# Optimization experiments

Hardware: AMD Instinct MI355X
Metric: run time of the kernel (lower is better)

The kernel has to match this reference:

```python
import jax, jax.numpy as jnp
import numpy as np

N = 150000      # active voxels
C = 64          # head input channels
KK = 9          # 3x3 kernel offsets
H = W = 700     # BEV feature map
BN_EPS = 1e-5
HEADS = [("heatmap", 3), ("center", 2), ("center_z", 1), ("dim", 3), ("rot", 2)]


def _build_neighbor_table(seed=0):
    """Submanifold 3x3 neighbor indices for N active voxels on an HxW grid.
    Entry -1 means the neighbor site is inactive (contributes zero)."""
    rng = np.random.default_rng(seed)
    flat = rng.choice(H * W, size=N, replace=False)
    ys, xs = flat // W, flat % W
    lut = np.full(H * W, -1, np.int64)
    lut[flat] = np.arange(N)
    nbr = np.full((N, KK), -1, np.int64)
    k = 0
    for dy in (-1, 0, 1):
        for dx in (-1, 0, 1):
            ny, nx = ys + dy, xs + dx
            valid = (ny >= 0) & (ny < H) & (nx >= 0) & (nx < W)
            nf = np.where(valid, ny * W + nx, 0)
            nbr[:, k] = np.where(valid, lut[nf], -1)
            k += 1
    return nbr


def setup_inputs() -> dict:
    key = jax.random.key(0)
    ks = jax.random.split(key, 2 + 2 * len(HEADS))
    inp = {
        "features": jax.random.normal(ks[0], (N, C), jnp.float32),
        "nbr_idx": jnp.asarray(_build_neighbor_table(), jnp.int32),
        # one 3x3 subm conv per head, stacked: [n_heads, 9, C_in, C_out]
        "W3": jax.random.normal(ks[1], (len(HEADS), KK, C, C), jnp.float32) * 0.05,
        "gamma": jnp.ones((len(HEADS), C), jnp.float32),
        "beta": jnp.zeros((len(HEADS), C), jnp.float32),
    }
    for i, (name, oc) in enumerate(HEADS):
        inp[f"W1_{name}"] = jax.random.normal(ks[2 + i], (C, oc), jnp.float32) * 0.001
        if name == "heatmap":
            inp[f"b1_{name}"] = jnp.full((oc,), -float(np.log((1 - 0.01) / 0.01)), jnp.float32)
        else:
            inp[f"b1_{name}"] = jnp.zeros((oc,), jnp.float32)
    return inp


def _forward(features, nbr_idx, W3, gamma, beta, W1s, b1s):
    valid = nbr_idx >= 0                                  # [N, 9]
    idx = jnp.where(valid, nbr_idx, 0)
    # gather active-neighbor features; missing neighbors -> zero (subm conv)
    gathered = features[idx] * valid[..., None].astype(features.dtype)  # [N, 9, C]
    # all heads share the same input sparse tensor -> batched gather-GEMM
    h = jnp.einsum('nkc,hkco->hno', gathered, W3)         # [n_heads, N, C]
    # BatchNorm1d (training-mode batch stats, biased var) + ReLU
    mean = h.mean(axis=1, keepdims=True)
    var = ((h - mean) ** 2).mean(axis=1, keepdims=True)
    hn = (h - mean) * jax.lax.rsqrt(var + BN_EPS)
    hn = jax.nn.relu(hn * gamma[:, None, :] + beta[:, None, :])
    # per-head 1x1 subm conv == linear on active features
    return tuple(hn[i] @ W1s[i] + b1s[i] for i in range(len(HEADS)))


def reference(features, nbr_idx, W3, gamma, beta,
              W1_heatmap, b1_heatmap, W1_center, b1_center,
              W1_center_z, b1_center_z, W1_dim, b1_dim, W1_rot, b1_rot):
    W1s = [W1_heatmap, W1_center, W1_center_z, W1_dim, W1_rot]
    b1s = [b1_heatmap, b1_center, b1_center_z, b1_dim, b1_rot]
    return _forward(features, nbr_idx, W3, gamma, beta, W1s, b1s)
```

## Files before the change

### kernel.cpp

```cpp
#include <hip/hip_runtime.h>

#define NVOX 150000
#define BM 128
#define MTILES 1172
#define SROW 150016
#define NCOL 320

typedef __attribute__((ext_vector_type(8))) short bf16x8;
typedef __attribute__((ext_vector_type(4))) float f32x4;

__device__ __forceinline__ unsigned short f2bf(float f) {
    unsigned u = __builtin_bit_cast(unsigned, f);
    u += 0x7fffu + ((u >> 16) & 1u);
    return (unsigned short)(u >> 16);
}

__device__ __forceinline__ void gld16(const void* g, void* l) {
    __builtin_amdgcn_global_load_lds(
        (const __attribute__((address_space(1))) unsigned int*)g,
        (__attribute__((address_space(3))) unsigned int*)l, 16, 0, 0);
}

__global__ void prep_feat(const float* __restrict__ src, unsigned short* __restrict__ dst) {
    int i = blockIdx.x * 256 + threadIdx.x;
    if (i < NVOX * 8) {
        const float* s = src + (size_t)i * 8;
        float4 a = *(const float4*)s;
        float4 b = *(const float4*)(s + 4);
        union { bf16x8 v; unsigned short u[8]; } r;
        r.u[0] = f2bf(a.x); r.u[1] = f2bf(a.y); r.u[2] = f2bf(a.z); r.u[3] = f2bf(a.w);
        r.u[4] = f2bf(b.x); r.u[5] = f2bf(b.y); r.u[6] = f2bf(b.z); r.u[7] = f2bf(b.w);
        *(bf16x8*)(dst + (size_t)i * 8) = r.v;
    } else if (i < NVOX * 8 + 8) {
        bf16x8 z = {0, 0, 0, 0, 0, 0, 0, 0};
        *(bf16x8*)(dst + (size_t)i * 8) = z;
    }
}

__global__ void prep_w3(const float* __restrict__ w3, unsigned short* __restrict__ bt,
                        float* __restrict__ stats) {
    int i = blockIdx.x * 256 + threadIdx.x;
    int h = i / 36864;
    int rem = i - h * 36864;
    int kk = rem >> 12;
    int c = (rem >> 6) & 63;
    int o = rem & 63;
    bt[(size_t)(((h * 9 + kk) * 8) + (c >> 3)) * 512 + o * 8 + (c & 7)] = f2bf(w3[i]);
    if (i < 2 * NCOL) stats[i] = 0.f;
}

__global__ __launch_bounds__(512, 2)
void gemm_kernel(const unsigned short* __restrict__ featB,
                 const unsigned short* __restrict__ Bt2,
                 const int* __restrict__ nbr,
                 unsigned short* __restrict__ hbuf,
                 float* __restrict__ stats,
                 float* __restrict__ partials) {
    __shared__ __align__(16) char smem[119296];
    constexpr int SB_OFF = 32768;
    constexpr int IDX_OFF = 114688;
    constexpr int SRED_OFF = 88064;

    int mtile = blockIdx.x;
    int m0 = mtile * BM;

    int tid = threadIdx.x;
    int w = tid >> 6, lane = tid & 63;
    int quad = lane >> 4, m16 = lane & 15;

    for (int lin = tid; lin < BM * 9; lin += 512) {
        int row = lin / 9, kkq = lin - row * 9;
        int v = -1;
        if (m0 + row < NVOX) v = nbr[(size_t)(m0 + row) * 9 + kkq];
        *(int*)(smem + IDX_OFF + (kkq * BM + row) * 4) = ((v < 0) ? NVOX : v) * 128;
    }
    __syncthreads();

    f32x4 acc[4][5];
#pragma unroll
    for (int mt = 0; mt < 4; ++mt)
#pragma unroll
        for (int nt = 0; nt < 5; ++nt)
            acc[mt][nt] = (f32x4){0.f, 0.f, 0.f, 0.f};

    const char* fb = (const char*)featB;
    const char* bt = (const char*)Bt2;
    char* sAb[2] = {smem, smem + 16384};
    char* sBb[2] = {smem + SB_OFF, smem + SB_OFF + 40960};

    int mrow = (w >> 2) * 64;
    int cbase = (w & 3) * 80;

    int rloc = lane >> 3, j = lane & 7;
    int jx = (j ^ rloc) * 16;

    int bsj[5], bdj[5];
#pragma unroll
    for (int jj = 0; jj < 5; ++jj) {
        int u = w * 5 + jj;
        int h = u >> 3, c16 = u & 7;
        bsj[jj] = (h * 72 + c16) * 1024 + lane * 16;
        bdj[jj] = (h * 8 + c16) * 1024;
    }
    int sBoff[5];
#pragma unroll
    for (int nt = 0; nt < 5; ++nt) {
        int c = cbase + nt * 16 + m16;
        sBoff[nt] = (c >> 6) * 8192 + (c & 63) * 16;
    }
    int aRow[4];
#pragma unroll
    for (int mt = 0; mt < 4; ++mt)
        aRow[mt] = (mrow + mt * 16 + m16) * 128;
    int axor = m16 & 7;

    auto stage = [&](int buf, int kk) {
        char* sA = sAb[buf];
        char* sB = sBb[buf];
        int off0 = *(const int*)(smem + IDX_OFF + (kk * BM + w * 16 + rloc) * 4);
        int off1 = *(const int*)(smem + IDX_OFF + (kk * BM + w * 16 + 8 + rloc) * 4);
        gld16(fb + off0 + jx, sA + w * 2048);
        gld16(fb + off1 + jx, sA + w * 2048 + 1024);
#pragma unroll
        for (int jj = 0; jj < 5; ++jj)
            gld16(bt + (size_t)(bsj[jj] + kk * 8192), sB + bdj[jj]);
    };

    stage(0, 0);

#pragma unroll
    for (int kk = 0; kk < 9; ++kk) {
        const int p = kk & 1;
        if (kk < 8) {
            stage(p ^ 1, kk + 1);
            asm volatile("s_waitcnt vmcnt(7)" ::: "memory");
        } else {
            asm volatile("s_waitcnt vmcnt(0)" ::: "memory");
        }
        asm volatile("s_barrier" ::: "memory");
        __builtin_amdgcn_sched_barrier(0);
        __builtin_amdgcn_s_setprio(1);
#pragma unroll
        for (int ks = 0; ks < 2; ++ks) {
            bf16x8 af[4], bf[5];
            int xq = ((ks * 4 + quad) ^ axor) * 16;
#pragma unroll
            for (int mt = 0; mt < 4; ++mt)
                af[mt] = *(const bf16x8*)(sAb[p] + aRow[mt] + xq);
#pragma unroll
            for (int nt = 0; nt < 5; ++nt)
                bf[nt] = *(const bf16x8*)(sBb[p] + sBoff[nt] + (ks * 4 + quad) * 1024);
#pragma unroll
            for (int mt = 0; mt < 4; ++mt)
#pragma unroll
                for (int nt = 0; nt < 5; ++nt)
                    acc[mt][nt] = __builtin_amdgcn_mfma_f32_16x16x32_bf16(
                        af[mt], bf[nt], acc[mt][nt], 0, 0, 0);
        }
        __builtin_amdgcn_s_setprio(0);
        __builtin_amdgcn_sched_barrier(0);
        asm volatile("s_barrier" ::: "memory");
    }

#pragma unroll
    for (int mt = 0; mt < 4; ++mt) {
#pragma unroll
        for (int nt = 0; nt < 5; ++nt) {
            int col = cbase + nt * 16 + m16;
            int row = mrow + mt * 16 + quad * 4;
            f32x4 v = acc[mt][nt];
            unsigned lo = (unsigned)f2bf(v.x) | ((unsigned)f2bf(v.y) << 16);
            unsigned hi = (unsigned)f2bf(v.z) | ((unsigned)f2bf(v.w) << 16);
            uint2 pk; pk.x = lo; pk.y = hi;
            *(uint2*)(smem + col * 272 + row * 2) = pk;
        }
    }
    __syncthreads();
#pragma unroll
    for (int it = 0; it < 20; ++it) {
        int col = it * 16 + (tid >> 5);
        int l32 = tid & 31;
        uint2 v = *(const uint2*)(smem + col * 272 + l32 * 8);
        *(uint2*)(hbuf + (size_t)col * SROW + m0 + l32 * 4) = v;
    }

    float s[5], ss[5];
#pragma unroll
    for (int nt = 0; nt < 5; ++nt) {
        float a = 0.f, b = 0.f;
#pragma unroll
        for (int mt = 0; mt < 4; ++mt) {
            f32x4 v = acc[mt][nt];
            a += v.x + v.y + v.z + v.w;
            b += v.x * v.x + v.y * v.y + v.z * v.z + v.w * v.w;
        }
        s[nt] = a; ss[nt] = b;
        s[nt] += __shfl_xor(s[nt], 16); s[nt] += __shfl_xor(s[nt], 32);
        ss[nt] += __shfl_xor(ss[nt], 16); ss[nt] += __shfl_xor(ss[nt], 32);
    }
    if (quad == 0) {
#pragma unroll
        for (int nt = 0; nt < 5; ++nt) {
            float* p = (float*)(smem + SRED_OFF + (w * 80 + nt * 16 + m16) * 8);
            p[0] = s[nt]; p[1] = ss[nt];
        }
    }
    __syncthreads();
    if (tid < NCOL) {
        int c = tid;
        int qq = c / 80, lc = c - qq * 80;
        const float* p0 = (const float*)(smem + SRED_OFF + (qq * 80 + lc) * 8);
        const float* p1 = (const float*)(smem + SRED_OFF + ((qq + 4) * 80 + lc) * 8);
        float vsum = p0[0] + p1[0];
        float vss  = p0[1] + p1[1];
        if (partials) {
            float* pp = partials + (size_t)mtile * (2 * NCOL);
            pp[c] = vsum;
            pp[NCOL + c] = vss;
        } else {
            atomicAdd(&stats[c], vsum);
            atomicAdd(&stats[NCOL + c], vss);
        }
    }
}

__global__ __launch_bounds__(256)
void stats_reduce(const float* __restrict__ partials, float* __restrict__ stats) {
    __shared__ float red[256];
    int b = blockIdx.x;
    int tid = threadIdx.x;
    int cl = tid & 31;
    int chunk = tid >> 5;
    int jcol = b * 32 + cl;
    float s = 0.f;
    int m1 = chunk * 147 + 147; if (m1 > MTILES) m1 = MTILES;
    for (int m = chunk * 147; m < m1; ++m)
        s += partials[(size_t)m * (2 * NCOL) + jcol];
    red[tid] = s;
    __syncthreads();
    if (tid < 32) {
        float a = red[tid];
#pragma unroll
        for (int k = 1; k < 8; ++k) a += red[k * 32 + tid];
        stats[b * 32 + tid] = a;
    }
}

__global__ __launch_bounds__(256)
void head_kernel(const unsigned short* __restrict__ hbuf,
                 const float* __restrict__ stats,
                 const float* __restrict__ gamma, const float* __restrict__ beta,
                 const float* __restrict__ W1_0, const float* __restrict__ W1_1,
                 const float* __restrict__ W1_2, const float* __restrict__ W1_3,
                 const float* __restrict__ W1_4,
                 const float* __restrict__ b1_0, const float* __restrict__ b1_1,
                 const float* __restrict__ b1_2, const float* __restrict__ b1_3,
                 const float* __restrict__ b1_4,
                 float* __restrict__ out) {
    __shared__ float sScale[64], sShift[64], sW1[192], sB1[3];
    int h = blockIdx.y;
    const float* W1; const float* b1; int oc; size_t obase;
    if (h == 0)      { W1 = W1_0; b1 = b1_0; oc = 3; obase = 0; }
    else if (h == 1) { W1 = W1_1; b1 = b1_1; oc = 2; obase = 450000; }
    else if (h == 2) { W1 = W1_2; b1 = b1_2; oc = 1; obase = 750000; }
    else if (h == 3) { W1 = W1_3; b1 = b1_3; oc = 3; obase = 900000; }
    else             { W1 = W1_4; b1 = b1_4; oc = 2; obase = 1350000; }

    int tid = threadIdx.x;
    if (tid < 64) {
        int c = h * 64 + tid;
        float mean = stats[c] * (1.f / (float)NVOX);
        float var = stats[NCOL + c] * (1.f / (float)NVOX) - mean * mean;
        float inv = rsqrtf(var + 1e-5f);
        float sc = inv * gamma[c];
        sScale[tid] = sc;
        sShift[tid] = beta[c] - mean * sc;
    }
    for (int i = tid; i < 192; i += 256) {
        int cc = i / 3, jj = i - cc * 3;
        sW1[i] = (jj < oc) ? W1[cc * oc + jj] : 0.f;
    }
    if (tid == 0) {
        sB1[0] = b1[0];
        sB1[1] = (oc >= 2) ? b1[1] : 0.f;
        sB1[2] = (oc >= 3) ? b1[2] : 0.f;
    }
    __syncthreads();

    int n = (blockIdx.x * 256 + tid) * 4;
    if (n >= NVOX) return;
    const unsigned short* hp = hbuf + (size_t)(h * 64) * SROW + n;
    float x[4][3];
#pragma unroll
    for (int rr = 0; rr < 4; ++rr) { x[rr][0] = sB1[0]; x[rr][1] = sB1[1]; x[rr][2] = sB1[2]; }
#pragma unroll 8
    for (int cc = 0; cc < 64; ++cc) {
        uint2 raw = *(const uint2*)(hp + (size_t)cc * SROW);
        float sc = sScale[cc], sh = sShift[cc];
        float w0 = sW1[cc * 3 + 0], w1 = sW1[cc * 3 + 1], w2 = sW1[cc * 3 + 2];
        float v0 = __builtin_bit_cast(float, raw.x << 16);
        float v1 = __builtin_bit_cast(float, raw.x & 0xffff0000u);
        float v2 = __builtin_bit_cast(float, raw.y << 16);
        float v3 = __builtin_bit_cast(float, raw.y & 0xffff0000u);
        v0 = fmaxf(v0 * sc + sh, 0.f); v1 = fmaxf(v1 * sc + sh, 0.f);
        v2 = fmaxf(v2 * sc + sh, 0.f); v3 = fmaxf(v3 * sc + sh, 0.f);
        x[0][0] += v0 * w0; x[0][1] += v0 * w1; x[0][2] += v0 * w2;
        x[1][0] += v1 * w0; x[1][1] += v1 * w1; x[1][2] += v1 * w2;
        x[2][0] += v2 * w0; x[2][1] += v2 * w1; x[2][2] += v2 * w2;
        x[3][0] += v3 * w0; x[3][1] += v3 * w1; x[3][2] += v3 * w2;
    }
#pragma unroll
    for (int rr = 0; rr < 4; ++rr) {
        float* op = out + obase + (size_t)(n + rr) * oc;
        op[0] = x[rr][0];
        if (oc >= 2) op[1] = x[rr][1];
        if (oc >= 3) op[2] = x[rr][2];
    }
}

extern "C" void kernel_launch(void* const* d_in, const int* in_sizes, int n_in,
                              void* d_out, int out_size, void* d_ws, size_t ws_size,
                              hipStream_t stream) {
    const float* features = (const float*)d_in[0];
    const int* nbr        = (const int*)d_in[1];
    const float* w3       = (const float*)d_in[2];
    const float* gamma    = (const float*)d_in[3];
    const float* beta     = (const float*)d_in[4];
    const float* W1_0 = (const float*)d_in[5];  const float* b1_0 = (const float*)d_in[6];
    const float* W1_1 = (const float*)d_in[7];  const float* b1_1 = (const float*)d_in[8];
    const float* W1_2 = (const float*)d_in[9];  const float* b1_2 = (const float*)d_in[10];
    const float* W1_3 = (const float*)d_in[11]; const float* b1_3 = (const float*)d_in[12];
    const float* W1_4 = (const float*)d_in[13]; const float* b1_4 = (const float*)d_in[14];
    float* out = (float*)d_out;

    char* ws = (char*)d_ws;
    unsigned short* featB = (unsigned short*)ws;
    unsigned short* Bt2   = (unsigned short*)(ws + 19200128);
    float* stats          = (float*)(ws + 19568768);
    unsigned short* hbuf  = (unsigned short*)(ws + 19571328);
    constexpr size_t PART_OFF = 19571328 + (size_t)NCOL * SROW * 2;
    float* partials = nullptr;
    if (ws_size >= PART_OFF + (size_t)MTILES * 2 * NCOL * 4)
        partials = (float*)(ws + PART_OFF);

    prep_feat<<<(NVOX * 8 + 8 + 255) / 256, 256, 0, stream>>>(features, featB);
    prep_w3<<<184320 / 256, 256, 0, stream>>>(w3, Bt2, stats);
    gemm_kernel<<<MTILES, 512, 0, stream>>>(featB, Bt2, nbr, hbuf, stats, partials);
    if (partials)
        stats_reduce<<<20, 256, 0, stream>>>(partials, stats);
    head_kernel<<<dim3(147, 5), 256, 0, stream>>>(hbuf, stats, gamma, beta,
        W1_0, W1_1, W1_2, W1_3, W1_4, b1_0, b1_1, b1_2, b1_3, b1_4, out);
}
```

Baseline: 250.8 us.

## Triple-buffer gathered A tiles, merge prep kernels, and parallelize stats reduction

The GEMM kernel now keeps three LDS buffers for the gathered feature tiles, so neighbor gathers are issued two steps ahead while the weight tiles stay double-buffered. This deepens prefetch to hide random-gather latency, at the cost of 16 KB more LDS per block, which may reduce occupancy at two blocks per CU. The two prep kernels are merged into one launch. stats_reduce now runs on a 20x8 grid and combines results with atomicAdd, relying on stats being zeroed in prep.

```diff
diff --git a/kernel.cpp b/kernel.cpp
--- a/kernel.cpp
+++ b/kernel.cpp
@@ -21,32 +21,34 @@
         (__attribute__((address_space(3))) unsigned int*)l, 16, 0, 0);
 }
 
-__global__ void prep_feat(const float* __restrict__ src, unsigned short* __restrict__ dst) {
-    int i = blockIdx.x * 256 + threadIdx.x;
-    if (i < NVOX * 8) {
-        const float* s = src + (size_t)i * 8;
-        float4 a = *(const float4*)s;
-        float4 b = *(const float4*)(s + 4);
-        union { bf16x8 v; unsigned short u[8]; } r;
-        r.u[0] = f2bf(a.x); r.u[1] = f2bf(a.y); r.u[2] = f2bf(a.z); r.u[3] = f2bf(a.w);
-        r.u[4] = f2bf(b.x); r.u[5] = f2bf(b.y); r.u[6] = f2bf(b.z); r.u[7] = f2bf(b.w);
-        *(bf16x8*)(dst + (size_t)i * 8) = r.v;
-    } else if (i < NVOX * 8 + 8) {
-        bf16x8 z = {0, 0, 0, 0, 0, 0, 0, 0};
-        *(bf16x8*)(dst + (size_t)i * 8) = z;
-    }
-}
-
-__global__ void prep_w3(const float* __restrict__ w3, unsigned short* __restrict__ bt,
-                        float* __restrict__ stats) {
-    int i = blockIdx.x * 256 + threadIdx.x;
-    int h = i / 36864;
-    int rem = i - h * 36864;
-    int kk = rem >> 12;
-    int c = (rem >> 6) & 63;
-    int o = rem & 63;
-    bt[(size_t)(((h * 9 + kk) * 8) + (c >> 3)) * 512 + o * 8 + (c & 7)] = f2bf(w3[i]);
-    if (i < 2 * NCOL) stats[i] = 0.f;
+__global__ void prep_all(const float* __restrict__ src, unsigned short* __restrict__ dst,
+                         const float* __restrict__ w3, unsigned short* __restrict__ bt,
+                         float* __restrict__ stats) {
+    int bid = blockIdx.x, tid = threadIdx.x;
+    if (bid < 4688) {
+        int i = bid * 256 + tid;
+        if (i < NVOX * 8) {
+            const float* s = src + (size_t)i * 8;
+            float4 a = *(const float4*)s;
+            float4 b = *(const float4*)(s + 4);
+            union { bf16x8 v; unsigned short u[8]; } r;
+            r.u[0] = f2bf(a.x); r.u[1] = f2bf(a.y); r.u[2] = f2bf(a.z); r.u[3] = f2bf(a.w);
+            r.u[4] = f2bf(b.x); r.u[5] = f2bf(b.y); r.u[6] = f2bf(b.z); r.u[7] = f2bf(b.w);
+            *(bf16x8*)(dst + (size_t)i * 8) = r.v;
+        } else if (i < NVOX * 8 + 8) {
+            bf16x8 z = {0, 0, 0, 0, 0, 0, 0, 0};
+            *(bf16x8*)(dst + (size_t)i * 8) = z;
+        }
+    } else {
+        int i = (bid - 4688) * 256 + tid;
+        int h = i / 36864;
+        int rem = i - h * 36864;
+        int kk = rem >> 12;
+        int c = (rem >> 6) & 63;
+        int o = rem & 63;
+        bt[(size_t)(((h * 9 + kk) * 8) + (c >> 3)) * 512 + o * 8 + (c & 7)] = f2bf(w3[i]);
+        if (i < 2 * NCOL) stats[i] = 0.f;
+    }
 }
 
 __global__ __launch_bounds__(512, 2)
@@ -56,9 +58,9 @@
                  unsigned short* __restrict__ hbuf,
                  float* __restrict__ stats,
                  float* __restrict__ partials) {
-    __shared__ __align__(16) char smem[119296];
-    constexpr int SB_OFF = 32768;
-    constexpr int IDX_OFF = 114688;
+    __shared__ __align__(16) char smem[135680];
+    constexpr int SB_OFF = 49152;
+    constexpr int IDX_OFF = 131072;
     constexpr int SRED_OFF = 88064;
 
     int mtile = blockIdx.x;
@@ -85,8 +87,6 @@
 
     const char* fb = (const char*)featB;
     const char* bt = (const char*)Bt2;
-    char* sAb[2] = {smem, smem + 16384};
-    char* sBb[2] = {smem + SB_OFF, smem + SB_OFF + 40960};
 
     int mrow = (w >> 2) * 64;
     int cbase = (w & 3) * 80;
@@ -114,42 +114,32 @@
         aRow[mt] = (mrow + mt * 16 + m16) * 128;
     int axor = m16 & 7;
 
-    auto stage = [&](int buf, int kk) {
-        char* sA = sAb[buf];
-        char* sB = sBb[buf];
+    auto stageA = [&](int buf, int kk) {
+        char* sA = smem + buf * 16384;
         int off0 = *(const int*)(smem + IDX_OFF + (kk * BM + w * 16 + rloc) * 4);
         int off1 = *(const int*)(smem + IDX_OFF + (kk * BM + w * 16 + 8 + rloc) * 4);
         gld16(fb + off0 + jx, sA + w * 2048);
         gld16(fb + off1 + jx, sA + w * 2048 + 1024);
+    };
+    auto stageB = [&](int buf, int kk) {
+        char* sB = smem + SB_OFF + buf * 40960;
 #pragma unroll
         for (int jj = 0; jj < 5; ++jj)
             gld16(bt + (size_t)(bsj[jj] + kk * 8192), sB + bdj[jj]);
     };
-
-    stage(0, 0);
-
-#pragma unroll
-    for (int kk = 0; kk < 9; ++kk) {
-        const int p = kk & 1;
-        if (kk < 8) {
-            stage(p ^ 1, kk + 1);
-            asm volatile("s_waitcnt vmcnt(7)" ::: "memory");
-        } else {
-            asm volatile("s_waitcnt vmcnt(0)" ::: "memory");
-        }
-        asm volatile("s_barrier" ::: "memory");
-        __builtin_amdgcn_sched_barrier(0);
-        __builtin_amdgcn_s_setprio(1);
+    auto computeStep = [&](int pA, int pB) {
+        const char* sA = smem + pA * 16384;
+        const char* sB = smem + SB_OFF + pB * 40960;
 #pragma unroll
         for (int ks = 0; ks < 2; ++ks) {
             bf16x8 af[4], bf[5];
             int xq = ((ks * 4 + quad) ^ axor) * 16;
 #pragma unroll
             for (int mt = 0; mt < 4; ++mt)
-                af[mt] = *(const bf16x8*)(sAb[p] + aRow[mt] + xq);
+                af[mt] = *(const bf16x8*)(sA + aRow[mt] + xq);
 #pragma unroll
             for (int nt = 0; nt < 5; ++nt)
-                bf[nt] = *(const bf16x8*)(sBb[p] + sBoff[nt] + (ks * 4 + quad) * 1024);
+                bf[nt] = *(const bf16x8*)(sB + sBoff[nt] + (ks * 4 + quad) * 1024);
 #pragma unroll
             for (int mt = 0; mt < 4; ++mt)
 #pragma unroll
@@ -157,10 +147,41 @@
                     acc[mt][nt] = __builtin_amdgcn_mfma_f32_16x16x32_bf16(
                         af[mt], bf[nt], acc[mt][nt], 0, 0, 0);
         }
-        __builtin_amdgcn_s_setprio(0);
-        __builtin_amdgcn_sched_barrier(0);
-        asm volatile("s_barrier" ::: "memory");
-    }
+    };
+
+    stageA(0, 0);
+    stageA(1, 1);
+    stageB(0, 0);
+
+#define STR2(x) #x
+#define VMCNT(N) asm volatile("s_waitcnt vmcnt(" STR2(N) ")" ::: "memory")
+#define GEMM_STEP(KK, WN)                                                   \
+    do {                                                                    \
+        if ((KK) < 8) stageB((KK + 1) & 1, (KK) + 1);                       \
+        if ((KK) < 7) stageA(((KK) + 2) % 3, (KK) + 2);                     \
+        VMCNT(WN);                                                          \
+        asm volatile("s_barrier" ::: "memory");                             \
+        __builtin_amdgcn_sched_barrier(0);                                  \
+        __builtin_amdgcn_s_setprio(1);                                      \
+        computeStep((KK) % 3, (KK) & 1);                                    \
+        __builtin_amdgcn_s_setprio(0);                                      \
+        __builtin_amdgcn_sched_barrier(0);                                  \
+        asm volatile("s_barrier" ::: "memory");                             \
+    } while (0)
+
+    GEMM_STEP(0, 7);
+    GEMM_STEP(1, 9);
+    GEMM_STEP(2, 9);
+    GEMM_STEP(3, 9);
+    GEMM_STEP(4, 9);
+    GEMM_STEP(5, 9);
+    GEMM_STEP(6, 9);
+    GEMM_STEP(7, 7);
+    GEMM_STEP(8, 0);
+#undef GEMM_STEP
+#undef VMCNT
+#undef STR2
+    __builtin_amdgcn_sched_barrier(0);
 
 #pragma unroll
     for (int mt = 0; mt < 4; ++mt) {
@@ -227,14 +248,15 @@
 __global__ __launch_bounds__(256)
 void stats_reduce(const float* __restrict__ partials, float* __restrict__ stats) {
     __shared__ float red[256];
-    int b = blockIdx.x;
     int tid = threadIdx.x;
-    int cl = tid & 31;
-    int chunk = tid >> 5;
-    int jcol = b * 32 + cl;
+    int cl = tid & 31, sc = tid >> 5;
+    int jcol = blockIdx.x * 32 + cl;
+    int ybase = blockIdx.y * 147;
+    int mlo = ybase + sc * 19;
+    int mhi = ybase + 147; if (mhi > MTILES) mhi = MTILES;
+    int mend = mlo + 19; if (mend > mhi) mend = mhi;
     float s = 0.f;
-    int m1 = chunk * 147 + 147; if (m1 > MTILES) m1 = MTILES;
-    for (int m = chunk * 147; m < m1; ++m)
+    for (int m = mlo; m < mend; ++m)
         s += partials[(size_t)m * (2 * NCOL) + jcol];
     red[tid] = s;
     __syncthreads();
@@ -242,7 +264,7 @@
         float a = red[tid];
 #pragma unroll
         for (int k = 1; k < 8; ++k) a += red[k * 32 + tid];
-        stats[b * 32 + tid] = a;
+        atomicAdd(&stats[blockIdx.x * 32 + tid], a);
     }
 }
 
@@ -343,11 +365,10 @@
     if (ws_size >= PART_OFF + (size_t)MTILES * 2 * NCOL * 4)
         partials = (float*)(ws + PART_OFF);
 
-    prep_feat<<<(NVOX * 8 + 8 + 255) / 256, 256, 0, stream>>>(features, featB);
-    prep_w3<<<184320 / 256, 256, 0, stream>>>(w3, Bt2, stats);
+    prep_all<<<4688 + 720, 256, 0, stream>>>(features, featB, w3, Bt2, stats);
     gemm_kernel<<<MTILES, 512, 0, stream>>>(featB, Bt2, nbr, hbuf, stats, partials);
     if (partials)
-        stats_reduce<<<20, 256, 0, stream>>>(partials, stats);
+        stats_reduce<<<dim3(20, 8), 256, 0, stream>>>(partials, stats);
     head_kernel<<<dim3(147, 5), 256, 0, stream>>>(hbuf, stats, gamma, beta,
         W1_0, W1_1, W1_2, W1_3, W1_4, b1_0, b1_1, b1_2, b1_3, b1_4, out);
 }
```

New measurement: 208.7 us. 1.2x faster.
